# Optimization experiments

Measured on AMD Instinct MI355X. Metric: run time of the kernel, lower is better.

Reference implementation:

```python
import jax, jax.numpy as jnp
import numpy as np
from jax import lax

B, IN, H, OUT, M, R = 16384, 512, 1024, 512, 8, 256


def setup_inputs() -> dict:
    key = jax.random.key(0)
    ks = jax.random.split(key, 14)
    s = lambda *sh: 1.0 / np.sqrt(sh[-2] if len(sh) > 1 else sh[-1])
    return {
        "x": jax.random.normal(ks[0], (B, IN), jnp.float32),
        "W_in": jax.random.normal(ks[1], (IN, H), jnp.float32) * (1.0 / np.sqrt(IN)),
        "b_in": jnp.zeros((H,), jnp.float32),
        "W_mod": jax.random.normal(ks[2], (M, H, H), jnp.float32) * (1.0 / np.sqrt(H)),
        "b_mod": jnp.zeros((M, H), jnp.float32),
        "Wr1": jax.random.normal(ks[3], (H, R), jnp.float32) * (1.0 / np.sqrt(H)),
        "br1": jnp.zeros((R,), jnp.float32),
        "Wr2": jax.random.normal(ks[4], (R, M), jnp.float32) * (1.0 / np.sqrt(R)),
        "br2": jnp.zeros((M,), jnp.float32),
        "Wc": jax.random.normal(ks[5], (1, H), jnp.float32),
        "bc": jnp.zeros((H,), jnp.float32),
        "W_out": jax.random.normal(ks[6], (H, OUT), jnp.float32) * (1.0 / np.sqrt(H)),
        "b_out": jnp.zeros((OUT,), jnp.float32),
        "max_cycles": 4,
    }


def reference(x, W_in, b_in, W_mod, b_mod, Wr1, br1, Wr2, br2, Wc, bc, W_out, b_out, max_cycles):
    h = x @ W_in + b_in                      # [B, H]
    orig = h

    def body(h, c):
        # cycle_projection: Linear(1, H) applied to scalar cycle index c
        cycle_proj = c * Wc[0] + bc          # [H]
        r = jax.nn.relu((orig * cycle_proj) @ Wr1 + br1)   # [B, R]
        probs = jax.nn.softmax(r @ Wr2 + br2, axis=-1)     # [B, M]
        # all experts as one batched GEMM: [B,H] x [M,H,H] -> [B,M,H]
        expert = jax.nn.relu(jnp.einsum('bh,mhd->bmd', h, W_mod) + b_mod)
        h_new = jnp.einsum('bmd,bm->bd', expert, probs)    # softmax-weighted sum
        return h_new, None

    h, _ = lax.scan(body, h, jnp.arange(max_cycles, dtype=x.dtype))
    return h @ W_out + b_out                 # [B, OUT]
```

## Files before the change

### kernel.cpp

```cpp
#include <hip/hip_runtime.h>


typedef _Float16 half8 __attribute__((ext_vector_type(8)));
typedef _Float16 half4v __attribute__((ext_vector_type(4)));
typedef float floatx4 __attribute__((ext_vector_type(4)));

#define DEVI __device__ __forceinline__
#define CHUNK 8192

DEVI void async16(void* lds, const void* g) {
  __builtin_amdgcn_global_load_lds(
      (const __attribute__((address_space(1))) unsigned int*)g,
      (__attribute__((address_space(3))) unsigned int*)lds, 16, 0, 0);
}

DEVI floatx4 mfma_f16(half8 a, half8 b, floatx4 c) {
  return __builtin_amdgcn_mfma_f32_16x16x32_f16(a, b, c, 0, 0, 0);
}


__global__ __launch_bounds__(256) void k_cast16(const float* __restrict__ in,
                                                _Float16* __restrict__ o,
                                                int n4) {
  int i = blockIdx.x * 256 + threadIdx.x;
  if (i >= n4) return;
  float4 v = ((const float4*)in)[i];
  half4v h;
  h[0] = (_Float16)v.x;
  h[1] = (_Float16)v.y;
  h[2] = (_Float16)v.z;
  h[3] = (_Float16)v.w;
  ((half4v*)o)[i] = h;
}

__global__ __launch_bounds__(256) void k_transpose16(
    const float* __restrict__ in, const float* __restrict__ scale,
    _Float16* __restrict__ o, int R, int C) {
  __shared__ float tile[64][65];
  __shared__ float srow[64];
  int b = blockIdx.z;
  int r0 = blockIdx.y * 64, c0 = blockIdx.x * 64;
  const float* src = in + (size_t)b * R * C;
  int t = threadIdx.x;
  int lr = t >> 4;
  int lc4 = (t & 15) * 4;
#pragma unroll
  for (int rr = 0; rr < 64; rr += 16) {
    float4 v = *(const float4*)&src[(size_t)(r0 + lr + rr) * C + c0 + lc4];
    tile[lr + rr][lc4 + 0] = v.x;
    tile[lr + rr][lc4 + 1] = v.y;
    tile[lr + rr][lc4 + 2] = v.z;
    tile[lr + rr][lc4 + 3] = v.w;
  }
  if (t < 64) srow[t] = scale ? scale[r0 + t] : 1.0f;
  __syncthreads();
  int oc = t >> 2;
  int orr = (t & 3) * 16;
  alignas(16) _Float16 hv[16];
#pragma unroll
  for (int k = 0; k < 16; k++)
    hv[k] = (_Float16)(tile[orr + k][oc] * srow[orr + k]);
  size_t ob = (size_t)b * C * R + (size_t)(c0 + oc) * R + (r0 + orr);
  ((int4*)&o[ob])[0] = ((int4*)hv)[0];
  ((int4*)&o[ob])[1] = ((int4*)hv)[1];
}


__global__ __launch_bounds__(256) void k_gemm_f16(
    const _Float16* __restrict__ A, const _Float16* __restrict__ Bt,
    const float* __restrict__ bias, _Float16* __restrict__ O, int M, int N,
    int K) {
  __shared__ _Float16 sA[128 * 32], sB[128 * 32];
  int t = threadIdx.x, lane = t & 63, wave = t >> 6;
  int wr = wave >> 1, wc = wave & 1;
  int row0 = blockIdx.y * 128, col0 = blockIdx.x * 128;
  floatx4 acc[4][4];
  for (int i = 0; i < 4; i++)
    for (int j = 0; j < 4; j++) acc[i][j] = (floatx4){0.f, 0.f, 0.f, 0.f};
  int rr0 = t >> 2, kk0 = (t & 3) * 8;
  int ar = (lane & 15) * 32 + (lane >> 4) * 8;
  for (int k0 = 0; k0 < K; k0 += 32) {
    __syncthreads();
    async16(&sA[t * 8], &A[(size_t)(row0 + rr0) * K + k0 + kk0]);
    async16(&sA[(t + 256) * 8], &A[(size_t)(row0 + rr0 + 64) * K + k0 + kk0]);
    async16(&sB[t * 8], &Bt[(size_t)(col0 + rr0) * K + k0 + kk0]);
    async16(&sB[(t + 256) * 8], &Bt[(size_t)(col0 + rr0 + 64) * K + k0 + kk0]);
    __syncthreads();
    half8 a[4], b[4];
#pragma unroll
    for (int i = 0; i < 4; i++) {
      a[i] = *(const half8*)&sA[(wr * 64 + i * 16) * 32 + ar];
      b[i] = *(const half8*)&sB[(wc * 64 + i * 16) * 32 + ar];
    }
#pragma unroll
    for (int i = 0; i < 4; i++)
#pragma unroll
      for (int j = 0; j < 4; j++) acc[i][j] = mfma_f16(a[i], b[j], acc[i][j]);
  }
#pragma unroll
  for (int i = 0; i < 4; i++) {
    int rowb = row0 + wr * 64 + i * 16 + ((lane >> 4) << 2);
#pragma unroll
    for (int j = 0; j < 4; j++) {
      int col = col0 + wc * 64 + j * 16 + (lane & 15);
      float bv = bias ? bias[col] : 0.0f;
#pragma unroll
      for (int r = 0; r < 4; r++)
        O[(size_t)(rowb + r) * N + col] = (_Float16)(acc[i][j][r] + bv);
    }
  }
}

__global__ __launch_bounds__(256) void k_gemm_f32(
    const _Float16* __restrict__ A, const _Float16* __restrict__ Bt,
    const float* __restrict__ bias, float* __restrict__ O, int M, int N,
    int K) {
  __shared__ _Float16 sA[128 * 32], sB[128 * 32];
  int t = threadIdx.x, lane = t & 63, wave = t >> 6;
  int wr = wave >> 1, wc = wave & 1;
  int row0 = blockIdx.y * 128, col0 = blockIdx.x * 128;
  floatx4 acc[4][4];
  for (int i = 0; i < 4; i++)
    for (int j = 0; j < 4; j++) acc[i][j] = (floatx4){0.f, 0.f, 0.f, 0.f};
  int rr0 = t >> 2, kk0 = (t & 3) * 8;
  int ar = (lane & 15) * 32 + (lane >> 4) * 8;
  for (int k0 = 0; k0 < K; k0 += 32) {
    __syncthreads();
    async16(&sA[t * 8], &A[(size_t)(row0 + rr0) * K + k0 + kk0]);
    async16(&sA[(t + 256) * 8], &A[(size_t)(row0 + rr0 + 64) * K + k0 + kk0]);
    async16(&sB[t * 8], &Bt[(size_t)(col0 + rr0) * K + k0 + kk0]);
    async16(&sB[(t + 256) * 8], &Bt[(size_t)(col0 + rr0 + 64) * K + k0 + kk0]);
    __syncthreads();
    half8 a[4], b[4];
#pragma unroll
    for (int i = 0; i < 4; i++) {
      a[i] = *(const half8*)&sA[(wr * 64 + i * 16) * 32 + ar];
      b[i] = *(const half8*)&sB[(wc * 64 + i * 16) * 32 + ar];
    }
#pragma unroll
    for (int i = 0; i < 4; i++)
#pragma unroll
      for (int j = 0; j < 4; j++) acc[i][j] = mfma_f16(a[i], b[j], acc[i][j]);
  }
#pragma unroll
  for (int i = 0; i < 4; i++) {
    int rowb = row0 + wr * 64 + i * 16 + ((lane >> 4) << 2);
#pragma unroll
    for (int j = 0; j < 4; j++) {
      int col = col0 + wc * 64 + j * 16 + (lane & 15);
      float bv = bias ? bias[col] : 0.0f;
#pragma unroll
      for (int r = 0; r < 4; r++)
        O[(size_t)(rowb + r) * N + col] = acc[i][j][r] + bv;
    }
  }
}


__global__ __launch_bounds__(256) void k_router4(
    const float* __restrict__ PQ, const float* __restrict__ br1,
    const float* __restrict__ Wr2, const float* __restrict__ br2,
    float* __restrict__ probs, int B) {
  int lane = threadIdx.x & 63;
  int wave = threadIdx.x >> 6;
  int row = blockIdx.x * 4 + wave;
  float cval = (float)blockIdx.y;
  float4 p4 = ((const float4*)(PQ + (size_t)row * 512))[lane];
  float4 q4 = ((const float4*)(PQ + (size_t)row * 512 + 256))[lane];
  float4 b4 = ((const float4*)br1)[lane];
  float rv[4];
  rv[0] = fmaxf(cval * p4.x + q4.x + b4.x, 0.f);
  rv[1] = fmaxf(cval * p4.y + q4.y + b4.y, 0.f);
  rv[2] = fmaxf(cval * p4.z + q4.z + b4.z, 0.f);
  rv[3] = fmaxf(cval * p4.w + q4.w + b4.w, 0.f);
  float lg[8] = {0.f, 0.f, 0.f, 0.f, 0.f, 0.f, 0.f, 0.f};
#pragma unroll
  for (int k = 0; k < 4; k++) {
    const float4* w = (const float4*)(Wr2 + (size_t)(lane * 4 + k) * 8);
    float4 w0 = w[0], w1 = w[1];
    lg[0] += rv[k] * w0.x;
    lg[1] += rv[k] * w0.y;
    lg[2] += rv[k] * w0.z;
    lg[3] += rv[k] * w0.w;
    lg[4] += rv[k] * w1.x;
    lg[5] += rv[k] * w1.y;
    lg[6] += rv[k] * w1.z;
    lg[7] += rv[k] * w1.w;
  }
#pragma unroll
  for (int s = 32; s > 0; s >>= 1)
#pragma unroll
    for (int m = 0; m < 8; m++) lg[m] += __shfl_xor(lg[m], s);
#pragma unroll
  for (int m = 0; m < 8; m++) lg[m] += br2[m];
  float mx = lg[0];
#pragma unroll
  for (int m = 1; m < 8; m++) mx = fmaxf(mx, lg[m]);
  float e[8];
  float sum = 0.f;
#pragma unroll
  for (int m = 0; m < 8; m++) {
    e[m] = expf(lg[m] - mx);
    sum += e[m];
  }
  float inv = 1.f / sum;
  if (lane < 8)
    probs[(size_t)blockIdx.y * B * 8 + (size_t)row * 8 + lane] = e[lane] * inv;
}


__global__ __launch_bounds__(512, 2) void k_expert_pair(
    const _Float16* __restrict__ hin, const _Float16* __restrict__ WT,
    const float* __restrict__ bmod, const float* __restrict__ probs,
    _Float16* __restrict__ part, int rowbase) {
  __shared__ _Float16 sA[256 * 32];
  __shared__ _Float16 sB[2 * 128 * 32];
  __shared__ float sProb[2 * 256];
  __shared__ float sBias[2 * 128];
  const int K = 1024;
  int t = threadIdx.x, lane = t & 63, wave = t >> 6;
  int wr = wave >> 1;
  int wc = wave & 1;
  int z = blockIdx.z;
  int col0 = blockIdx.x * 128;
  int prow0 = blockIdx.y * 256;
  int grow0 = rowbase + prow0;
  if (t < 512) {
    int e = t >> 8, r = t & 255;
    sProb[t] = probs[(size_t)(grow0 + r) * 8 + z + e * 4];
  }
  if (t < 256) {
    int e = t >> 7, cc = t & 127;
    sBias[t] = bmod[(size_t)(z + e * 4) * 1024 + col0 + cc];
  }
  const _Float16* B0 = WT + (size_t)z * 1024 * 1024;
  const _Float16* B1 = WT + (size_t)(z + 4) * 1024 * 1024;
  floatx4 acc0[4][4], acc1[4][4];
#pragma unroll
  for (int i = 0; i < 4; i++)
#pragma unroll
    for (int j = 0; j < 4; j++) {
      acc0[i][j] = (floatx4){0.f, 0.f, 0.f, 0.f};
      acc1[i][j] = (floatx4){0.f, 0.f, 0.f, 0.f};
    }
  int rr0 = t >> 2, kk0 = (t & 3) * 8;
  int ar = (lane & 15) * 32 + (lane >> 4) * 8;
  for (int k0 = 0; k0 < K; k0 += 32) {
    __syncthreads();
    async16(&sA[t * 8], &hin[(size_t)(grow0 + rr0) * K + k0 + kk0]);
    async16(&sA[(t + 512) * 8],
            &hin[(size_t)(grow0 + rr0 + 128) * K + k0 + kk0]);
    async16(&sB[t * 8], &B0[(size_t)(col0 + rr0) * K + k0 + kk0]);
    async16(&sB[(t + 512) * 8], &B1[(size_t)(col0 + rr0) * K + k0 + kk0]);
    __syncthreads();
    half8 a[4], b0[4], b1[4];
#pragma unroll
    for (int i = 0; i < 4; i++) {
      a[i] = *(const half8*)&sA[(wr * 64 + i * 16) * 32 + ar];
      b0[i] = *(const half8*)&sB[(wc * 64 + i * 16) * 32 + ar];
      b1[i] = *(const half8*)&sB[4096 + (wc * 64 + i * 16) * 32 + ar];
    }
#pragma unroll
    for (int i = 0; i < 4; i++)
#pragma unroll
      for (int j = 0; j < 4; j++) {
        acc0[i][j] = mfma_f16(a[i], b0[j], acc0[i][j]);
        acc1[i][j] = mfma_f16(a[i], b1[j], acc1[i][j]);
      }
  }
#pragma unroll
  for (int i = 0; i < 4; i++) {
    int lr0 = wr * 64 + i * 16 + ((lane >> 4) << 2);
    float p0[4], p1[4];
#pragma unroll
    for (int r = 0; r < 4; r++) {
      p0[r] = sProb[lr0 + r];
      p1[r] = sProb[256 + lr0 + r];
    }
#pragma unroll
    for (int j = 0; j < 4; j++) {
      int cl = wc * 64 + j * 16 + (lane & 15);
      float bb0 = sBias[cl];
      float bb1 = sBias[128 + cl];
      size_t base =
          (size_t)z * CHUNK * 1024 + (size_t)(prow0 + lr0) * 1024 + col0 + cl;
#pragma unroll
      for (int r = 0; r < 4; r++) {
        float v = p0[r] * fmaxf(acc0[i][j][r] + bb0, 0.f) +
                  p1[r] * fmaxf(acc1[i][j][r] + bb1, 0.f);
        part[base + (size_t)r * 1024] = (_Float16)v;
      }
    }
  }
}

__global__ __launch_bounds__(256) void k_combine4(
    const _Float16* __restrict__ part, _Float16* __restrict__ hout,
    int rowbase) {
  const size_t S = (size_t)CHUNK * 1024;
  size_t i = ((size_t)blockIdx.x * 256 + threadIdx.x) * 8;
  float s[8] = {0.f, 0.f, 0.f, 0.f, 0.f, 0.f, 0.f, 0.f};
#pragma unroll
  for (int m = 0; m < 4; m++) {
    half8 v = *(const half8*)&part[(size_t)m * S + i];
#pragma unroll
    for (int k = 0; k < 8; k++) s[k] += (float)v[k];
  }
  half8 o;
#pragma unroll
  for (int k = 0; k < 8; k++) o[k] = (_Float16)s[k];
  *(half8*)&hout[(size_t)rowbase * 1024 + i] = o;
}


extern "C" void kernel_launch(void* const* d_in, const int* in_sizes, int n_in,
                              void* d_out, int out_size, void* d_ws,
                              size_t ws_size, hipStream_t stream) {
  (void)in_sizes;
  (void)n_in;
  (void)out_size;
  (void)ws_size;
  const float* x = (const float*)d_in[0];
  const float* W_in = (const float*)d_in[1];
  const float* b_in = (const float*)d_in[2];
  const float* W_mod = (const float*)d_in[3];
  const float* b_mod = (const float*)d_in[4];
  const float* Wr1 = (const float*)d_in[5];
  const float* br1 = (const float*)d_in[6];
  const float* Wr2 = (const float*)d_in[7];
  const float* br2 = (const float*)d_in[8];
  const float* Wc = (const float*)d_in[9];
  const float* bc = (const float*)d_in[10];
  const float* W_out = (const float*)d_in[11];
  const float* b_out = (const float*)d_in[12];
  float* out = (float*)d_out;

  const int B = 16384, IN = 512, H = 1024, OUT = 512, M = 8, R = 256;
  const size_t MB = 1024 * 1024;

  char* p = (char*)d_ws;
  _Float16* partial = (_Float16*)(p + 0);
  _Float16* xh = (_Float16*)(p + 0);
  _Float16* WinT = (_Float16*)(p + 64 * MB);
  _Float16* W1T = (_Float16*)(p + 65 * MB);
  _Float16* WoutT = (_Float16*)(p + 66 * MB);
  _Float16* WmodT = (_Float16*)(p + 67 * MB);
  _Float16* origHi = (_Float16*)(p + 83 * MB);
  _Float16* hA = (_Float16*)(p + 115 * MB);
  _Float16* hB = (_Float16*)(p + 147 * MB);
  float* PQ = (float*)(p + 179 * MB);
  float* probs4 = (float*)(p + 211 * MB);

  k_cast16<<<dim3(B * IN / 4 / 256), dim3(256), 0, stream>>>(x, xh,
                                                             B * IN / 4);
  k_transpose16<<<dim3(H / 64, IN / 64, 1), dim3(256), 0, stream>>>(
      W_in, nullptr, WinT, IN, H);
  k_transpose16<<<dim3(R / 64, H / 64, 1), dim3(256), 0, stream>>>(
      Wr1, Wc, W1T, H, R);
  k_transpose16<<<dim3(R / 64, H / 64, 1), dim3(256), 0, stream>>>(
      Wr1, bc, W1T + (size_t)R * H, H, R);
  k_transpose16<<<dim3(OUT / 64, H / 64, 1), dim3(256), 0, stream>>>(
      W_out, nullptr, WoutT, H, OUT);
  k_transpose16<<<dim3(H / 64, H / 64, M), dim3(256), 0, stream>>>(
      W_mod, nullptr, WmodT, H, H);

  k_gemm_f16<<<dim3(H / 128, B / 128), dim3(256), 0, stream>>>(
      xh, WinT, b_in, origHi, B, H, IN);
  k_gemm_f32<<<dim3(2 * R / 128, B / 128), dim3(256), 0, stream>>>(
      origHi, W1T, nullptr, PQ, B, 2 * R, H);
  k_router4<<<dim3(B / 4, 4), dim3(256), 0, stream>>>(PQ, br1, Wr2, br2,
                                                      probs4, B);

  const _Float16* hcur = origHi;
  _Float16* hbufs[2] = {hA, hB};
  for (int c = 0; c < 4; c++) {
    const float* probs = probs4 + (size_t)c * B * 8;
    _Float16* hn = hbufs[c & 1];
    for (int chunk = 0; chunk < 2; chunk++) {
      int rowbase = chunk * CHUNK;
      k_expert_pair<<<dim3(H / 128, CHUNK / 256, 4), dim3(512), 0, stream>>>(
          hcur, WmodT, b_mod, probs, partial, rowbase);
      k_combine4<<<dim3(CHUNK * 1024 / (256 * 8)), dim3(256), 0, stream>>>(
          partial, hn, rowbase);
    }
    hcur = hn;
  }

  k_gemm_f32<<<dim3(OUT / 128, B / 128), dim3(256), 0, stream>>>(
      hcur, WoutT, b_out, out, B, OUT, H);
}
```

Baseline: 1.758 ms.

## Double-buffer LDS tiles in expert GEMM to overlap global loads with MFMA

Splits the A and B shared-memory tiles of the paired-expert GEMM into two buffers. The first K-slice is prefetched before the loop, and each iteration issues async global-to-LDS loads for the next slice while computing on the current one. This drops one of the two barriers per iteration and aims to hide global load latency behind MFMA work. It doubles LDS use for the tiles. The overlap depends on the compiler not inserting a full vmcnt wait before the LDS reads.

New measurement: 1.752 ms. Within noise of the previous version (-0.3%).

```diff
diff --git a/kernel.cpp b/kernel.cpp
--- a/kernel.cpp
+++ b/kernel.cpp
@@ -213,8 +213,8 @@
     const _Float16* __restrict__ hin, const _Float16* __restrict__ WT,
     const float* __restrict__ bmod, const float* __restrict__ probs,
     _Float16* __restrict__ part, int rowbase) {
-  __shared__ _Float16 sA[256 * 32];
-  __shared__ _Float16 sB[2 * 128 * 32];
+  __shared__ _Float16 sA[2][256 * 32];
+  __shared__ _Float16 sB[2][2 * 128 * 32];
   __shared__ float sProb[2 * 256];
   __shared__ float sBias[2 * 128];
   const int K = 1024;
@@ -225,7 +225,7 @@
   int col0 = blockIdx.x * 128;
   int prow0 = blockIdx.y * 256;
   int grow0 = rowbase + prow0;
-  if (t < 512) {
+  {
     int e = t >> 8, r = t & 255;
     sProb[t] = probs[(size_t)(grow0 + r) * 8 + z + e * 4];
   }
@@ -245,20 +245,29 @@
     }
   int rr0 = t >> 2, kk0 = (t & 3) * 8;
   int ar = (lane & 15) * 32 + (lane >> 4) * 8;
+  const size_t aoff0 = (size_t)(grow0 + rr0) * K + kk0;
+  const size_t aoff1 = (size_t)(grow0 + rr0 + 128) * K + kk0;
+  const size_t boff = (size_t)(col0 + rr0) * K + kk0;
+  async16(&sA[0][t * 8], &hin[aoff0]);
+  async16(&sA[0][(t + 512) * 8], &hin[aoff1]);
+  async16(&sB[0][t * 8], &B0[boff]);
+  async16(&sB[0][(t + 512) * 8], &B1[boff]);
   for (int k0 = 0; k0 < K; k0 += 32) {
+    int cur = (k0 >> 5) & 1;
     __syncthreads();
-    async16(&sA[t * 8], &hin[(size_t)(grow0 + rr0) * K + k0 + kk0]);
-    async16(&sA[(t + 512) * 8],
-            &hin[(size_t)(grow0 + rr0 + 128) * K + k0 + kk0]);
-    async16(&sB[t * 8], &B0[(size_t)(col0 + rr0) * K + k0 + kk0]);
-    async16(&sB[(t + 512) * 8], &B1[(size_t)(col0 + rr0) * K + k0 + kk0]);
-    __syncthreads();
+    if (k0 + 32 < K) {
+      int nxt = 1 - cur;
+      async16(&sA[nxt][t * 8], &hin[aoff0 + k0 + 32]);
+      async16(&sA[nxt][(t + 512) * 8], &hin[aoff1 + k0 + 32]);
+      async16(&sB[nxt][t * 8], &B0[boff + k0 + 32]);
+      async16(&sB[nxt][(t + 512) * 8], &B1[boff + k0 + 32]);
+    }
     half8 a[4], b0[4], b1[4];
 #pragma unroll
     for (int i = 0; i < 4; i++) {
-      a[i] = *(const half8*)&sA[(wr * 64 + i * 16) * 32 + ar];
-      b0[i] = *(const half8*)&sB[(wc * 64 + i * 16) * 32 + ar];
-      b1[i] = *(const half8*)&sB[4096 + (wc * 64 + i * 16) * 32 + ar];
+      a[i] = *(const half8*)&sA[cur][(wr * 64 + i * 16) * 32 + ar];
+      b0[i] = *(const half8*)&sB[cur][(wc * 64 + i * 16) * 32 + ar];
+      b1[i] = *(const half8*)&sB[cur][4096 + (wc * 64 + i * 16) * 32 + ar];
     }
 #pragma unroll
     for (int i = 0; i < 4; i++)
```
